# Kernel tuning notes

Hardware: AMD Instinct MI355X
Metric: run time of the kernel (lower is better)

The kernel has to match this reference:

```python
import jax, jax.numpy as jnp
import numpy as np

N = 50000      # nodes
E = 800000     # edges (avg degree 16)
F_IN = 128     # input feature dim
HID = 128      # 2 * out_classes
OUT = 64       # out_classes


def setup_inputs() -> dict:
    key = jax.random.key(0)
    ks = jax.random.split(key, 12)
    x = jax.random.normal(ks[0], (N, F_IN), jnp.float32)
    edge_index = jax.random.randint(ks[1], (2, E), 0, N, jnp.int32)
    def lin(k, fi, fo):
        return jax.random.normal(k, (fi, fo), jnp.float32) / np.float32(np.sqrt(fi))
    return {
        "x": x,
        "edge_index": edge_index,
        "W1": lin(ks[2], F_IN, HID), "b1": jnp.zeros((HID,), jnp.float32),
        "W2": lin(ks[3], HID, HID),  "b2": jnp.zeros((HID,), jnp.float32),
        "W3": lin(ks[4], HID, HID),  "b3": jnp.zeros((HID,), jnp.float32),
        "jk_w": jax.random.normal(ks[5], (3,), jnp.float32),
        "fc_W": lin(ks[6], HID, OUT), "fc_b": jnp.zeros((OUT,), jnp.float32),
    }


def _gcn_conv(h, W, b, row, col, n):
    """PyG GCNConv: linear -> add self-loops -> sym-normalized aggregate -> bias."""
    h = h @ W                                        # [n, d_out]
    loops = jnp.arange(n, dtype=row.dtype)
    r = jnp.concatenate([row, loops])                # sources
    c = jnp.concatenate([col, loops])                # targets
    deg = jax.ops.segment_sum(jnp.ones_like(c, h.dtype), c, num_segments=n)
    dinv = jnp.where(deg > 0, jax.lax.rsqrt(deg), 0.0)
    norm = dinv[r] * dinv[c]                         # [E+n]
    msg = h[r] * norm[:, None]                       # gather + scale
    return jax.ops.segment_sum(msg, c, num_segments=n) + b


def _neighbor_mean(h, row, col, n):
    """sample_neighbors with scale_factor=2: exact mean over out-neighbors,
    own feature when degree == 0 (top-k branch is provably dead code)."""
    s = jax.ops.segment_sum(h[col], row, num_segments=n)
    deg = jax.ops.segment_sum(jnp.ones_like(row, h.dtype), row, num_segments=n)
    mean = s / jnp.maximum(deg, 1.0)[:, None]
    return jnp.where((deg > 0)[:, None], mean, h)


def reference(x, edge_index, W1, b1, W2, b2, W3, b3, jk_w, fc_W, fc_b):
    row, col = edge_index[0], edge_index[1]
    n = x.shape[0]
    # layer 0: GCN -> ReLU -> (dropout: eval identity) -> neighbor sampling
    h0 = jax.nn.relu(_gcn_conv(x, W1, b1, row, col, n))
    h0 = _neighbor_mean(h0, row, col, n)
    # layer 1: GCN -> ReLU; historical-activation update is identity on first call
    h1 = jax.nn.relu(_gcn_conv(h0, W2, b2, row, col, n))
    # layer 2
    h2 = jax.nn.relu(_gcn_conv(h1, W3, b3, row, col, n))
    # dynamic JK aggregation
    w = jax.nn.softmax(jk_w)
    h = w[0] * h0 + w[1] * h1 + w[2] * h2
    return h @ fc_W + fc_b
```

## Files before the change

### kernel.cpp

```cpp
#include <hip/hip_runtime.h>
#include <stdint.h>

typedef unsigned int  uint32;
typedef unsigned short u16;

typedef short bfx8 __attribute__((ext_vector_type(8)));
typedef float f32x4 __attribute__((ext_vector_type(4)));
typedef float f32x2 __attribute__((ext_vector_type(2)));

#define NBP 256
#define CH  2048
#define BS  4608

__device__ __forceinline__ float b2f(u16 u) {
    union { uint32 i; float f; } v; v.i = ((uint32)u) << 16; return v.f;
}
__device__ __forceinline__ u16 f2b(float f) {
    union { float f; uint32 i; } v; v.f = f;
    uint32 u = v.i;
    return (u16)((u + 0x7fffu + ((u >> 16) & 1u)) >> 16);
}
__device__ __forceinline__ float blo(uint32 u) {
    union { uint32 i; float f; } v; v.i = u << 16; return v.f;
}
__device__ __forceinline__ float bhi(uint32 u) {
    union { uint32 i; float f; } v; v.i = u & 0xffff0000u; return v.f;
}
__device__ __forceinline__ uint32 packbf(float a, float b) {
    return (uint32)f2b(a) | ((uint32)f2b(b) << 16);
}
__device__ __forceinline__ void splitf(float x, u16& h, u16& l) {
    h = f2b(x);
    l = f2b(x - b2f(h));
}

__global__ __launch_bounds__(256) void k_init(
    int* __restrict__ curC, int* __restrict__ curR,
    const float* __restrict__ W1, const float* __restrict__ W2,
    const float* __restrict__ W3, const float* __restrict__ fcW,
    u16* __restrict__ WTh, u16* __restrict__ WTl, int WTN) {
    int t = threadIdx.x;
    if (blockIdx.x == 0) {
        curC[t] = t * BS;
        curR[t] = t * BS;
        return;
    }
    int i = ((int)blockIdx.x - 1) * 256 + t;
    if (i >= WTN) return;
    float w;
    if (i < 3 * 16384) {
        int m = i >> 14, j = i & 16383;
        int fo = j >> 7, fi = j & 127;
        const float* W = (m == 0) ? W1 : (m == 1) ? W2 : W3;
        w = W[fi * 128 + fo];
    } else {
        int j = i - 3 * 16384;
        int fo = j >> 7, fi = j & 127;
        w = fcW[fi * 64 + fo];
    }
    u16 h, l; splitf(w, h, l);
    WTh[i] = h; WTl[i] = l;
}

__global__ __launch_bounds__(256) void k_partC(
    const int* __restrict__ row, const int* __restrict__ col, int E,
    int* __restrict__ curC, int* __restrict__ curR,
    uint32* __restrict__ partC, uint32* __restrict__ partR) {
    __shared__ uint32 stagedC[CH], stagedR[CH];
    __shared__ int hp[NBP], expk[NBP], curp[NBP], runC[NBP], runR[NBP];
    __shared__ int wsum[4];
    int t = threadIdx.x;
    int lane = t & 63, wid = t >> 6;
    int base = blockIdx.x * CH;
    int n = E - base; if (n > CH) n = CH;

    int er[8], ec[8];
#pragma unroll
    for (int j = 0; j < 8; ++j) {
        int i = t + j * 256;
        if (i < n) { er[j] = row[base + i]; ec[j] = col[base + i]; }
        else er[j] = -1;
    }
    hp[t] = 0;
    __syncthreads();
#pragma unroll
    for (int j = 0; j < 8; ++j) {
        if (er[j] >= 0) {
            atomicAdd(&hp[ec[j] >> 8], 1);
            atomicAdd(&hp[er[j] >> 8], 0x10000);
        }
    }
    __syncthreads();
    int v = hp[t];
    int x = v;
#pragma unroll
    for (int d = 1; d < 64; d <<= 1) {
        int u = __shfl_up(x, d);
        if (lane >= d) x += u;
    }
    if (lane == 63) wsum[wid] = x;
    __syncthreads();
    int add = 0;
    for (int i = 0; i < wid; ++i) add += wsum[i];
    int ex = x + add - v;
    expk[t] = ex;
    curp[t] = ex;
    int vC = v & 0xffff, vR = v >> 16;
    runC[t] = vC ? atomicAdd(&curC[t], vC) : 0;
    runR[t] = vR ? atomicAdd(&curR[t], vR) : 0;
    __syncthreads();
#pragma unroll
    for (int j = 0; j < 8; ++j) {
        if (er[j] >= 0) {
            int cb = ec[j] >> 8, rb = er[j] >> 8;
            int pC = atomicAdd(&curp[cb], 1) & 0xffff;
            stagedC[pC] = ((uint32)ec[j] << 16) | (uint32)er[j];
            int pR = atomicAdd(&curp[rb], 0x10000) >> 16;
            stagedR[pR] = ((uint32)er[j] << 16) | (uint32)ec[j];
        }
    }
    __syncthreads();
    for (int i = t; i < n; i += 256) {
        uint32 pv = stagedC[i];
        int b = pv >> 24;
        partC[runC[b] + (i - (expk[b] & 0xffff))] = pv;
    }
    for (int i = t; i < n; i += 256) {
        uint32 pv = stagedR[i];
        int b = pv >> 24;
        partR[runR[b] + (i - (expk[b] >> 16))] = pv;
    }
}

__global__ __launch_bounds__(256) void k_fillD(
    const uint32* __restrict__ partC, const uint32* __restrict__ partR,
    const int* __restrict__ curC, const int* __restrict__ curR,
    int* __restrict__ off_in, int* __restrict__ end_in,
    int* __restrict__ off_out, int* __restrict__ end_out,
    u16* __restrict__ csr_src, u16* __restrict__ csr_dst,
    float* __restrict__ dinv, int NB, int N) {
    int part = ((int)blockIdx.x >= NB) ? 1 : 0;
    int b = (int)blockIdx.x - part * NB;
    const uint32* arr = part ? partR : partC;
    const int* curA   = part ? curR : curC;
    int* offA         = part ? off_out : off_in;
    int* endA         = part ? end_out : end_in;
    u16* csr          = part ? csr_dst : csr_src;
    int t = threadIdx.x;
    int lane = t & 63, wid = t >> 6;
    int base = b * BS, end = curA[b];
    __shared__ int cnt[NBP], cur[NBP];
    __shared__ int wsum[4];
    cnt[t] = 0;
    __syncthreads();
    for (int i = base + t; i < end; i += 256)
        atomicAdd(&cnt[(arr[i] >> 16) & 255], 1);
    __syncthreads();
    int v = cnt[t];
    int x = v;
#pragma unroll
    for (int d = 1; d < 64; d <<= 1) {
        int u = __shfl_up(x, d);
        if (lane >= d) x += u;
    }
    if (lane == 63) wsum[wid] = x;
    __syncthreads();
    int add = 0;
    for (int i = 0; i < wid; ++i) add += wsum[i];
    int ex = x + add - v;
    cur[t] = ex;
    int node = (b << 8) + t;
    if (node < N) {
        offA[node] = base + ex;
        endA[node] = base + ex + v;
        if (part == 0) dinv[node] = rsqrtf((float)(v + 1));
    }
    __syncthreads();
    for (int i = base + t; i < end; i += 256) {
        uint32 pv = arr[i];
        int local = (pv >> 16) & 255;
        int pos = atomicAdd(&cur[local], 1);
        csr[base + pos] = (u16)(pv & 0xffffu);
    }
}

__global__ __launch_bounds__(256) void k_gemm0(
    const float* __restrict__ A, const u16* __restrict__ WTh, const u16* __restrict__ WTl,
    const float* __restrict__ dinv, u16* __restrict__ G, int M) {
    const int lane = threadIdx.x & 63;
    const int q = lane >> 4, l = lane & 15;
    int rbase = blockIdx.x * 128 + (threadIdx.x >> 6) * 32;
    if (rbase >= M) return;
    int r0 = rbase + l;      if (r0 >= M) r0 = M - 1;
    int r1 = rbase + 16 + l; if (r1 >= M) r1 = M - 1;

    f32x4 acc[2][8];
#pragma unroll
    for (int i = 0; i < 2; ++i)
#pragma unroll
        for (int j = 0; j < 8; ++j) acc[i][j] = (f32x4){0.f, 0.f, 0.f, 0.f};

#pragma unroll
    for (int kc = 0; kc < 4; ++kc) {
        int k0 = kc * 32 + q * 8;
        bfx8 ah0, ah1;
        {
            f32x4 a = *(const f32x4*)(A + (size_t)r0 * 128 + k0);
            f32x4 b = *(const f32x4*)(A + (size_t)r0 * 128 + k0 + 4);
            float xx[8] = {a[0], a[1], a[2], a[3], b[0], b[1], b[2], b[3]};
#pragma unroll
            for (int j = 0; j < 8; ++j) ah0[j] = (short)f2b(xx[j]);
        }
        {
            f32x4 a = *(const f32x4*)(A + (size_t)r1 * 128 + k0);
            f32x4 b = *(const f32x4*)(A + (size_t)r1 * 128 + k0 + 4);
            float xx[8] = {a[0], a[1], a[2], a[3], b[0], b[1], b[2], b[3]};
#pragma unroll
            for (int j = 0; j < 8; ++j) ah1[j] = (short)f2b(xx[j]);
        }
#pragma unroll
        for (int ct = 0; ct < 8; ++ct) {
            bfx8 bh = *(const bfx8*)(WTh + (ct * 16 + l) * 128 + k0);
            bfx8 bl = *(const bfx8*)(WTl + (ct * 16 + l) * 128 + k0);
            acc[0][ct] = __builtin_amdgcn_mfma_f32_16x16x32_bf16(ah0, bh, acc[0][ct], 0, 0, 0);
            acc[0][ct] = __builtin_amdgcn_mfma_f32_16x16x32_bf16(ah0, bl, acc[0][ct], 0, 0, 0);
            acc[1][ct] = __builtin_amdgcn_mfma_f32_16x16x32_bf16(ah1, bh, acc[1][ct], 0, 0, 0);
            acc[1][ct] = __builtin_amdgcn_mfma_f32_16x16x32_bf16(ah1, bl, acc[1][ct], 0, 0, 0);
        }
    }
#pragma unroll
    for (int rs = 0; rs < 2; ++rs) {
#pragma unroll
        for (int rr = 0; rr < 4; ++rr) {
            int rw = rbase + rs * 16 + q * 4 + rr;
            if (rw < M) {
                float dv = dinv[rw];
#pragma unroll
                for (int ct = 0; ct < 8; ++ct)
                    G[(size_t)rw * 128 + ct * 16 + l] = f2b(acc[rs][ct][rr] * dv);
            }
        }
    }
}

__global__ __launch_bounds__(256) void k_gemm1p(
    const u16* __restrict__ Ah,
    const u16* __restrict__ WTh, const u16* __restrict__ WTl,
    const float* __restrict__ dinv, u16* __restrict__ G, int M) {
    const int lane = threadIdx.x & 63;
    const int q = lane >> 4, l = lane & 15;
    int rbase = blockIdx.x * 128 + (threadIdx.x >> 6) * 32;
    if (rbase >= M) return;
    int r0 = rbase + l;      if (r0 >= M) r0 = M - 1;
    int r1 = rbase + 16 + l; if (r1 >= M) r1 = M - 1;

    f32x4 acc[2][8];
#pragma unroll
    for (int i = 0; i < 2; ++i)
#pragma unroll
        for (int j = 0; j < 8; ++j) acc[i][j] = (f32x4){0.f, 0.f, 0.f, 0.f};

#pragma unroll
    for (int kc = 0; kc < 4; ++kc) {
        int k0 = kc * 32 + q * 8;
        bfx8 ah0 = *(const bfx8*)(Ah + (size_t)r0 * 128 + k0);
        bfx8 ah1 = *(const bfx8*)(Ah + (size_t)r1 * 128 + k0);
#pragma unroll
        for (int ct = 0; ct < 8; ++ct) {
            bfx8 bh = *(const bfx8*)(WTh + (ct * 16 + l) * 128 + k0);
            bfx8 bl = *(const bfx8*)(WTl + (ct * 16 + l) * 128 + k0);
            acc[0][ct] = __builtin_amdgcn_mfma_f32_16x16x32_bf16(ah0, bh, acc[0][ct], 0, 0, 0);
            acc[0][ct] = __builtin_amdgcn_mfma_f32_16x16x32_bf16(ah0, bl, acc[0][ct], 0, 0, 0);
            acc[1][ct] = __builtin_amdgcn_mfma_f32_16x16x32_bf16(ah1, bh, acc[1][ct], 0, 0, 0);
            acc[1][ct] = __builtin_amdgcn_mfma_f32_16x16x32_bf16(ah1, bl, acc[1][ct], 0, 0, 0);
        }
    }
#pragma unroll
    for (int rs = 0; rs < 2; ++rs) {
#pragma unroll
        for (int rr = 0; rr < 4; ++rr) {
            int rw = rbase + rs * 16 + q * 4 + rr;
            if (rw < M) {
                float dv = dinv[rw];
#pragma unroll
                for (int ct = 0; ct < 8; ++ct)
                    G[(size_t)rw * 128 + ct * 16 + l] = f2b(acc[rs][ct][rr] * dv);
            }
        }
    }
}

__global__ __launch_bounds__(256) void k_agg(
    const uint32* __restrict__ g, const u16* __restrict__ csr,
    const int* __restrict__ off, const int* __restrict__ endo,
    const float* __restrict__ dinv,
    const f32x2* __restrict__ bias, uint32* __restrict__ outH, int n) {
    int w = (blockIdx.x * 256 + threadIdx.x) >> 6;
    if (w >= n) return;
    int lane = threadIdx.x & 63;
    uint32 sv = g[(size_t)w * 64 + lane];
    float s0 = blo(sv), s1 = bhi(sv);
    int e = off[w], e1 = endo[w];
    for (; e + 16 <= e1; e += 16) {
        int ix[16];
#pragma unroll
        for (int j = 0; j < 16; ++j) ix[j] = csr[e + j];
        uint32 vv[16];
#pragma unroll
        for (int j = 0; j < 16; ++j) vv[j] = g[(size_t)ix[j] * 64 + lane];
#pragma unroll
        for (int j = 0; j < 16; ++j) { s0 += blo(vv[j]); s1 += bhi(vv[j]); }
    }
    for (; e + 4 <= e1; e += 4) {
        int ix[4];
#pragma unroll
        for (int j = 0; j < 4; ++j) ix[j] = csr[e + j];
        uint32 vv[4];
#pragma unroll
        for (int j = 0; j < 4; ++j) vv[j] = g[(size_t)ix[j] * 64 + lane];
#pragma unroll
        for (int j = 0; j < 4; ++j) { s0 += blo(vv[j]); s1 += bhi(vv[j]); }
    }
    for (; e < e1; ++e) {
        uint32 v = g[(size_t)csr[e] * 64 + lane];
        s0 += blo(v); s1 += bhi(v);
    }
    float dc = dinv[w];
    f32x2 bb = bias[lane];
    float o0 = fmaxf(fmaf(s0, dc, bb[0]), 0.f);
    float o1 = fmaxf(fmaf(s1, dc, bb[1]), 0.f);
    outH[(size_t)w * 64 + lane] = packbf(o0, o1);
}

__global__ __launch_bounds__(256) void k_mean(
    const uint32* __restrict__ h, const u16* __restrict__ csr,
    const int* __restrict__ off, const int* __restrict__ endo,
    uint32* __restrict__ outH, int n) {
    int w = (blockIdx.x * 256 + threadIdx.x) >> 6;
    if (w >= n) return;
    int lane = threadIdx.x & 63;
    int e = off[w], e1 = endo[w];
    int d = e1 - e;
    float s0 = 0.f, s1 = 0.f;
    for (; e + 16 <= e1; e += 16) {
        int ix[16];
#pragma unroll
        for (int j = 0; j < 16; ++j) ix[j] = csr[e + j];
        uint32 vv[16];
#pragma unroll
        for (int j = 0; j < 16; ++j) vv[j] = h[(size_t)ix[j] * 64 + lane];
#pragma unroll
        for (int j = 0; j < 16; ++j) { s0 += blo(vv[j]); s1 += bhi(vv[j]); }
    }
    for (; e + 4 <= e1; e += 4) {
        int ix[4];
#pragma unroll
        for (int j = 0; j < 4; ++j) ix[j] = csr[e + j];
        uint32 vv[4];
#pragma unroll
        for (int j = 0; j < 4; ++j) vv[j] = h[(size_t)ix[j] * 64 + lane];
#pragma unroll
        for (int j = 0; j < 4; ++j) { s0 += blo(vv[j]); s1 += bhi(vv[j]); }
    }
    for (; e < e1; ++e) {
        uint32 v = h[(size_t)csr[e] * 64 + lane];
        s0 += blo(v); s1 += bhi(v);
    }
    float o0, o1;
    if (d > 0) {
        float inv = 1.f / (float)d;
        o0 = s0 * inv; o1 = s1 * inv;
    } else {
        uint32 sv = h[(size_t)w * 64 + lane];
        o0 = blo(sv); o1 = bhi(sv);
    }
    outH[(size_t)w * 64 + lane] = packbf(o0, o1);
}

__global__ __launch_bounds__(256) void k_final(
    const u16* __restrict__ h0, const u16* __restrict__ h1,
    const u16* __restrict__ h2, const float* __restrict__ jkw,
    const u16* __restrict__ fcWTh, const u16* __restrict__ fcWTl,
    const float* __restrict__ fcb, float* __restrict__ out, int M) {
    float a0 = jkw[0], a1 = jkw[1], a2 = jkw[2];
    float mx = fmaxf(a0, fmaxf(a1, a2));
    float e0 = expf(a0 - mx), e1 = expf(a1 - mx), e2 = expf(a2 - mx);
    float inv = 1.f / (e0 + e1 + e2);
    float w0 = e0 * inv, w1 = e1 * inv, w2 = e2 * inv;

    const int lane = threadIdx.x & 63;
    const int q = lane >> 4, l = lane & 15;
    int rbase = blockIdx.x * 128 + (threadIdx.x >> 6) * 32;
    if (rbase >= M) return;
    int r0 = rbase + l;      if (r0 >= M) r0 = M - 1;
    int r1 = rbase + 16 + l; if (r1 >= M) r1 = M - 1;

    f32x4 acc[2][4];
#pragma unroll
    for (int i = 0; i < 2; ++i)
#pragma unroll
        for (int j = 0; j < 4; ++j) acc[i][j] = (f32x4){0.f, 0.f, 0.f, 0.f};

    union U8 { bfx8 v; u16 u[8]; };

#pragma unroll
    for (int kc = 0; kc < 4; ++kc) {
        int k0 = kc * 32 + q * 8;
        bfx8 ah[2];
        const int rr2[2] = {r0, r1};
#pragma unroll
        for (int half = 0; half < 2; ++half) {
            size_t o = (size_t)rr2[half] * 128 + k0;
            U8 x0, x1, x2, rh;
            x0.v = *(const bfx8*)(h0 + o);
            x1.v = *(const bfx8*)(h1 + o);
            x2.v = *(const bfx8*)(h2 + o);
#pragma unroll
            for (int j = 0; j < 8; ++j) {
                float c = w0 * b2f(x0.u[j]) + w1 * b2f(x1.u[j]) + w2 * b2f(x2.u[j]);
                rh.u[j] = f2b(c);
            }
            ah[half] = rh.v;
        }
#pragma unroll
        for (int ct = 0; ct < 4; ++ct) {
            bfx8 bh = *(const bfx8*)(fcWTh + (ct * 16 + l) * 128 + k0);
            bfx8 bl = *(const bfx8*)(fcWTl + (ct * 16 + l) * 128 + k0);
#pragma unroll
            for (int half = 0; half < 2; ++half) {
                acc[half][ct] = __builtin_amdgcn_mfma_f32_16x16x32_bf16(ah[half], bh, acc[half][ct], 0, 0, 0);
                acc[half][ct] = __builtin_amdgcn_mfma_f32_16x16x32_bf16(ah[half], bl, acc[half][ct], 0, 0, 0);
            }
        }
    }
#pragma unroll
    for (int rs = 0; rs < 2; ++rs) {
#pragma unroll
        for (int rr = 0; rr < 4; ++rr) {
            int rw = rbase + rs * 16 + q * 4 + rr;
            if (rw < M) {
#pragma unroll
                for (int ct = 0; ct < 4; ++ct) {
                    int cc = ct * 16 + l;
                    out[(size_t)rw * 64 + cc] = acc[rs][ct][rr] + fcb[cc];
                }
            }
        }
    }
}

extern "C" void kernel_launch(void* const* d_in, const int* in_sizes, int n_in,
                              void* d_out, int out_size, void* d_ws, size_t ws_size,
                              hipStream_t stream) {
    const int N = in_sizes[0] / 128;
    const int E = in_sizes[1] / 2;
    const int NB = (N + 255) >> 8;

    const float* x    = (const float*)d_in[0];
    const int* row    = (const int*)d_in[1];
    const int* col    = row + E;
    const float* W1   = (const float*)d_in[2];
    const float* b1   = (const float*)d_in[3];
    const float* W2   = (const float*)d_in[4];
    const float* b2   = (const float*)d_in[5];
    const float* W3   = (const float*)d_in[6];
    const float* b3   = (const float*)d_in[7];
    const float* jkw  = (const float*)d_in[8];
    const float* fcW  = (const float*)d_in[9];
    const float* fcb  = (const float*)d_in[10];
    float* outp       = (float*)d_out;

    char* ws = (char*)d_ws;
    size_t off = 0;
    auto alloc = [&](size_t bytes) -> char* {
        char* p = ws + off;
        off += (bytes + 255) & ~(size_t)255;
        return p;
    };
    int* curC   = (int*)alloc((size_t)NBP * sizeof(int));
    int* curR   = (int*)alloc((size_t)NBP * sizeof(int));
    int* off_in  = (int*)alloc((size_t)N * sizeof(int));
    int* end_in  = (int*)alloc((size_t)N * sizeof(int));
    int* off_out = (int*)alloc((size_t)N * sizeof(int));
    int* end_out = (int*)alloc((size_t)N * sizeof(int));
    uint32* partC = (uint32*)alloc((size_t)NBP * BS * sizeof(uint32));
    uint32* partR = (uint32*)alloc((size_t)NBP * BS * sizeof(uint32));
    u16* csr_src = (u16*)alloc((size_t)NBP * BS * sizeof(u16));
    u16* csr_dst = (u16*)alloc((size_t)NBP * BS * sizeof(u16));
    float* dinv  = (float*)alloc((size_t)N * sizeof(float));
    const int WTN = 3 * 16384 + 8192;
    u16* WTh = (u16*)alloc((size_t)WTN * sizeof(u16));
    u16* WTl = (u16*)alloc((size_t)WTN * sizeof(u16));
    size_t FB = (size_t)N * 128 * sizeof(u16);
    u16* gbuf = (u16*)alloc(FB);
    u16* t0   = (u16*)alloc(FB);
    u16* h0   = (u16*)alloc(FB);
    u16* h1   = (u16*)alloc(FB);
    u16* h2   = (u16*)alloc(FB);

    const int B = 256;
    int Gh = (E + CH - 1) / CH;
    int Gg = (N + 127) / 128;
    int Gwt = (WTN + B - 1) / B;

    k_init<<<1 + Gwt, B, 0, stream>>>(curC, curR, W1, W2, W3, fcW, WTh, WTl, WTN);
    k_partC<<<Gh, B, 0, stream>>>(row, col, E, curC, curR, partC, partR);
    k_fillD<<<2 * NB, B, 0, stream>>>(partC, partR, curC, curR,
                                      off_in, end_in, off_out, end_out,
                                      csr_src, csr_dst, dinv, NB, N);
    k_gemm0<<<Gg, B, 0, stream>>>(x, WTh, WTl, dinv, gbuf, N);

    int aggG = (N + 3) / 4;

    k_agg<<<aggG, B, 0, stream>>>((const uint32*)gbuf, csr_src, off_in, end_in, dinv,
                                  (const f32x2*)b1, (uint32*)t0, N);
    k_mean<<<aggG, B, 0, stream>>>((const uint32*)t0, csr_dst, off_out, end_out,
                                   (uint32*)h0, N);
    k_gemm1p<<<Gg, B, 0, stream>>>(h0, WTh + 16384, WTl + 16384, dinv, gbuf, N);
    k_agg<<<aggG, B, 0, stream>>>((const uint32*)gbuf, csr_src, off_in, end_in, dinv,
                                  (const f32x2*)b2, (uint32*)h1, N);
    k_gemm1p<<<Gg, B, 0, stream>>>(h1, WTh + 2 * 16384, WTl + 2 * 16384, dinv, gbuf, N);
    k_agg<<<aggG, B, 0, stream>>>((const uint32*)gbuf, csr_src, off_in, end_in, dinv,
                                  (const f32x2*)b3, (uint32*)h2, N);
    k_final<<<Gg, B, 0, stream>>>(h0, h1, h2, jkw,
                                  WTh + 3 * 16384, WTl + 3 * 16384, fcb, outp, N);
}
```

Baseline: 335.2 us.

## Fuse GCN aggregation with following GEMMs and merge setup kernels

Merges the weight-split init into the edge partition kernel and the first GEMM into the CSR fill kernel. The first GEMM runs concurrently with CSR construction, so it no longer scales by dinv; the first aggregation applies per-neighbor dinv instead. The mean, aggregation and final JK/fc steps are fused with the next layer's GEMM through a 16-row shared-memory tile, cutting the launch count and the round trips of intermediate features through memory. The cost is extra dinv gathers per edge in the first aggregation and small per-block GEMMs that reload weights in every block, plus a memset to zero the bucket cursors.

```diff
diff --git a/kernel.cpp b/kernel.cpp
--- a/kernel.cpp
+++ b/kernel.cpp
@@ -34,42 +34,35 @@
     l = f2b(x - b2f(h));
 }
 
-__global__ __launch_bounds__(256) void k_init(
+__global__ __launch_bounds__(256) void k_partC_ws(
+    const int* __restrict__ row, const int* __restrict__ col, int E, int Gh,
     int* __restrict__ curC, int* __restrict__ curR,
+    uint32* __restrict__ partC, uint32* __restrict__ partR,
     const float* __restrict__ W1, const float* __restrict__ W2,
     const float* __restrict__ W3, const float* __restrict__ fcW,
     u16* __restrict__ WTh, u16* __restrict__ WTl, int WTN) {
-    int t = threadIdx.x;
-    if (blockIdx.x == 0) {
-        curC[t] = t * BS;
-        curR[t] = t * BS;
-        return;
-    }
-    int i = ((int)blockIdx.x - 1) * 256 + t;
-    if (i >= WTN) return;
-    float w;
-    if (i < 3 * 16384) {
-        int m = i >> 14, j = i & 16383;
-        int fo = j >> 7, fi = j & 127;
-        const float* W = (m == 0) ? W1 : (m == 1) ? W2 : W3;
-        w = W[fi * 128 + fo];
-    } else {
-        int j = i - 3 * 16384;
-        int fo = j >> 7, fi = j & 127;
-        w = fcW[fi * 64 + fo];
-    }
-    u16 h, l; splitf(w, h, l);
-    WTh[i] = h; WTl[i] = l;
-}
-
-__global__ __launch_bounds__(256) void k_partC(
-    const int* __restrict__ row, const int* __restrict__ col, int E,
-    int* __restrict__ curC, int* __restrict__ curR,
-    uint32* __restrict__ partC, uint32* __restrict__ partR) {
     __shared__ uint32 stagedC[CH], stagedR[CH];
     __shared__ int hp[NBP], expk[NBP], curp[NBP], runC[NBP], runR[NBP];
     __shared__ int wsum[4];
     int t = threadIdx.x;
+    if ((int)blockIdx.x >= Gh) {
+        int i = ((int)blockIdx.x - Gh) * 256 + t;
+        if (i >= WTN) return;
+        float w;
+        if (i < 3 * 16384) {
+            int m = i >> 14, j = i & 16383;
+            int fo = j >> 7, fi = j & 127;
+            const float* W = (m == 0) ? W1 : (m == 1) ? W2 : W3;
+            w = W[fi * 128 + fo];
+        } else {
+            int j = i - 3 * 16384;
+            int fo = j >> 7, fi = j & 127;
+            w = fcW[fi * 64 + fo];
+        }
+        u16 h, l; splitf(w, h, l);
+        WTh[i] = h; WTl[i] = l;
+        return;
+    }
     int lane = t & 63, wid = t >> 6;
     int base = blockIdx.x * CH;
     int n = E - base; if (n > CH) n = CH;
@@ -106,8 +99,8 @@
     expk[t] = ex;
     curp[t] = ex;
     int vC = v & 0xffff, vR = v >> 16;
-    runC[t] = vC ? atomicAdd(&curC[t], vC) : 0;
-    runR[t] = vR ? atomicAdd(&curR[t], vR) : 0;
+    runC[t] = t * BS + (vC ? atomicAdd(&curC[t], vC) : 0);
+    runR[t] = t * BS + (vR ? atomicAdd(&curR[t], vR) : 0);
     __syncthreads();
 #pragma unroll
     for (int j = 0; j < 8; ++j) {
@@ -132,13 +125,70 @@
     }
 }
 
-__global__ __launch_bounds__(256) void k_fillD(
+__global__ __launch_bounds__(256) void k_fillD_g0(
     const uint32* __restrict__ partC, const uint32* __restrict__ partR,
     const int* __restrict__ curC, const int* __restrict__ curR,
     int* __restrict__ off_in, int* __restrict__ end_in,
     int* __restrict__ off_out, int* __restrict__ end_out,
     u16* __restrict__ csr_src, u16* __restrict__ csr_dst,
-    float* __restrict__ dinv, int NB, int N) {
+    float* __restrict__ dinv, int NB, int N,
+    const float* __restrict__ A, const u16* __restrict__ WTh,
+    const u16* __restrict__ WTl, u16* __restrict__ G) {
+    if ((int)blockIdx.x >= 2 * NB) {
+        int blk = (int)blockIdx.x - 2 * NB;
+        const int lane = threadIdx.x & 63;
+        const int q = lane >> 4, l = lane & 15;
+        int rbase = blk * 128 + (threadIdx.x >> 6) * 32;
+        if (rbase >= N) return;
+        int r0 = rbase + l;      if (r0 >= N) r0 = N - 1;
+        int r1 = rbase + 16 + l; if (r1 >= N) r1 = N - 1;
+        f32x4 acc[2][8];
+#pragma unroll
+        for (int i = 0; i < 2; ++i)
+#pragma unroll
+            for (int j = 0; j < 8; ++j) acc[i][j] = (f32x4){0.f, 0.f, 0.f, 0.f};
+#pragma unroll
+        for (int kc = 0; kc < 4; ++kc) {
+            int k0 = kc * 32 + q * 8;
+            bfx8 ah0, ah1;
+            {
+                f32x4 a = *(const f32x4*)(A + (size_t)r0 * 128 + k0);
+                f32x4 b = *(const f32x4*)(A + (size_t)r0 * 128 + k0 + 4);
+                float xx[8] = {a[0], a[1], a[2], a[3], b[0], b[1], b[2], b[3]};
+#pragma unroll
+                for (int j = 0; j < 8; ++j) ah0[j] = (short)f2b(xx[j]);
+            }
+            {
+                f32x4 a = *(const f32x4*)(A + (size_t)r1 * 128 + k0);
+                f32x4 b = *(const f32x4*)(A + (size_t)r1 * 128 + k0 + 4);
+                float xx[8] = {a[0], a[1], a[2], a[3], b[0], b[1], b[2], b[3]};
+#pragma unroll
+                for (int j = 0; j < 8; ++j) ah1[j] = (short)f2b(xx[j]);
+            }
+#pragma unroll
+            for (int ct = 0; ct < 8; ++ct) {
+                bfx8 bh = *(const bfx8*)(WTh + (ct * 16 + l) * 128 + k0);
+                bfx8 bl = *(const bfx8*)(WTl + (ct * 16 + l) * 128 + k0);
+                acc[0][ct] = __builtin_amdgcn_mfma_f32_16x16x32_bf16(ah0, bh, acc[0][ct], 0, 0, 0);
+                acc[0][ct] = __builtin_amdgcn_mfma_f32_16x16x32_bf16(ah0, bl, acc[0][ct], 0, 0, 0);
+                acc[1][ct] = __builtin_amdgcn_mfma_f32_16x16x32_bf16(ah1, bh, acc[1][ct], 0, 0, 0);
+                acc[1][ct] = __builtin_amdgcn_mfma_f32_16x16x32_bf16(ah1, bl, acc[1][ct], 0, 0, 0);
+            }
+        }
+#pragma unroll
+        for (int rs = 0; rs < 2; ++rs) {
+#pragma unroll
+            for (int rr = 0; rr < 4; ++rr) {
+                int rw = rbase + rs * 16 + q * 4 + rr;
+                if (rw < N) {
+#pragma unroll
+                    for (int ct = 0; ct < 8; ++ct)
+                        G[(size_t)rw * 128 + ct * 16 + l] = f2b(acc[rs][ct][rr]);
+                }
+            }
+        }
+        return;
+    }
     int part = ((int)blockIdx.x >= NB) ? 1 : 0;
     int b = (int)blockIdx.x - part * NB;
     const uint32* arr = part ? partR : partC;
@@ -148,7 +198,7 @@
     u16* csr          = part ? csr_dst : csr_src;
     int t = threadIdx.x;
     int lane = t & 63, wid = t >> 6;
-    int base = b * BS, end = curA[b];
+    int base = b * BS, end = base + curA[b];
     __shared__ int cnt[NBP], cur[NBP];
     __shared__ int wsum[4];
     cnt[t] = 0;
@@ -184,113 +234,7 @@
     }
 }
 
-__global__ __launch_bounds__(256) void k_gemm0(
-    const float* __restrict__ A, const u16* __restrict__ WTh, const u16* __restrict__ WTl,
-    const float* __restrict__ dinv, u16* __restrict__ G, int M) {
-    const int lane = threadIdx.x & 63;
-    const int q = lane >> 4, l = lane & 15;
-    int rbase = blockIdx.x * 128 + (threadIdx.x >> 6) * 32;
-    if (rbase >= M) return;
-    int r0 = rbase + l;      if (r0 >= M) r0 = M - 1;
-    int r1 = rbase + 16 + l; if (r1 >= M) r1 = M - 1;
-
-    f32x4 acc[2][8];
-#pragma unroll
-    for (int i = 0; i < 2; ++i)
-#pragma unroll
-        for (int j = 0; j < 8; ++j) acc[i][j] = (f32x4){0.f, 0.f, 0.f, 0.f};
-
-#pragma unroll
-    for (int kc = 0; kc < 4; ++kc) {
-        int k0 = kc * 32 + q * 8;
-        bfx8 ah0, ah1;
-        {
-            f32x4 a = *(const f32x4*)(A + (size_t)r0 * 128 + k0);
-            f32x4 b = *(const f32x4*)(A + (size_t)r0 * 128 + k0 + 4);
-            float xx[8] = {a[0], a[1], a[2], a[3], b[0], b[1], b[2], b[3]};
-#pragma unroll
-            for (int j = 0; j < 8; ++j) ah0[j] = (short)f2b(xx[j]);
-        }
-        {
-            f32x4 a = *(const f32x4*)(A + (size_t)r1 * 128 + k0);
-            f32x4 b = *(const f32x4*)(A + (size_t)r1 * 128 + k0 + 4);
-            float xx[8] = {a[0], a[1], a[2], a[3], b[0], b[1], b[2], b[3]};
-#pragma unroll
-            for (int j = 0; j < 8; ++j) ah1[j] = (short)f2b(xx[j]);
-        }
-#pragma unroll
-        for (int ct = 0; ct < 8; ++ct) {
-            bfx8 bh = *(const bfx8*)(WTh + (ct * 16 + l) * 128 + k0);
-            bfx8 bl = *(const bfx8*)(WTl + (ct * 16 + l) * 128 + k0);
-            acc[0][ct] = __builtin_amdgcn_mfma_f32_16x16x32_bf16(ah0, bh, acc[0][ct], 0, 0, 0);
-            acc[0][ct] = __builtin_amdgcn_mfma_f32_16x16x32_bf16(ah0, bl, acc[0][ct], 0, 0, 0);
-            acc[1][ct] = __builtin_amdgcn_mfma_f32_16x16x32_bf16(ah1, bh, acc[1][ct], 0, 0, 0);
-            acc[1][ct] = __builtin_amdgcn_mfma_f32_16x16x32_bf16(ah1, bl, acc[1][ct], 0, 0, 0);
-        }
-    }
-#pragma unroll
-    for (int rs = 0; rs < 2; ++rs) {
-#pragma unroll
-        for (int rr = 0; rr < 4; ++rr) {
-            int rw = rbase + rs * 16 + q * 4 + rr;
-            if (rw < M) {
-                float dv = dinv[rw];
-#pragma unroll
-                for (int ct = 0; ct < 8; ++ct)
-                    G[(size_t)rw * 128 + ct * 16 + l] = f2b(acc[rs][ct][rr] * dv);
-            }
-        }
-    }
-}
-
-__global__ __launch_bounds__(256) void k_gemm1p(
-    const u16* __restrict__ Ah,
-    const u16* __restrict__ WTh, const u16* __restrict__ WTl,
-    const float* __restrict__ dinv, u16* __restrict__ G, int M) {
-    const int lane = threadIdx.x & 63;
-    const int q = lane >> 4, l = lane & 15;
-    int rbase = blockIdx.x * 128 + (threadIdx.x >> 6) * 32;
-    if (rbase >= M) return;
-    int r0 = rbase + l;      if (r0 >= M) r0 = M - 1;
-    int r1 = rbase + 16 + l; if (r1 >= M) r1 = M - 1;
-
-    f32x4 acc[2][8];
-#pragma unroll
-    for (int i = 0; i < 2; ++i)
-#pragma unroll
-        for (int j = 0; j < 8; ++j) acc[i][j] = (f32x4){0.f, 0.f, 0.f, 0.f};
-
-#pragma unroll
-    for (int kc = 0; kc < 4; ++kc) {
-        int k0 = kc * 32 + q * 8;
-        bfx8 ah0 = *(const bfx8*)(Ah + (size_t)r0 * 128 + k0);
-        bfx8 ah1 = *(const bfx8*)(Ah + (size_t)r1 * 128 + k0);
-#pragma unroll
-        for (int ct = 0; ct < 8; ++ct) {
-            bfx8 bh = *(const bfx8*)(WTh + (ct * 16 + l) * 128 + k0);
-            bfx8 bl = *(const bfx8*)(WTl + (ct * 16 + l) * 128 + k0);
-            acc[0][ct] = __builtin_amdgcn_mfma_f32_16x16x32_bf16(ah0, bh, acc[0][ct], 0, 0, 0);
-            acc[0][ct] = __builtin_amdgcn_mfma_f32_16x16x32_bf16(ah0, bl, acc[0][ct], 0, 0, 0);
-            acc[1][ct] = __builtin_amdgcn_mfma_f32_16x16x32_bf16(ah1, bh, acc[1][ct], 0, 0, 0);
-            acc[1][ct] = __builtin_amdgcn_mfma_f32_16x16x32_bf16(ah1, bl, acc[1][ct], 0, 0, 0);
-        }
-    }
-#pragma unroll
-    for (int rs = 0; rs < 2; ++rs) {
-#pragma unroll
-        for (int rr = 0; rr < 4; ++rr) {
-            int rw = rbase + rs * 16 + q * 4 + rr;
-            if (rw < M) {
-                float dv = dinv[rw];
-#pragma unroll
-                for (int ct = 0; ct < 8; ++ct)
-                    G[(size_t)rw * 128 + ct * 16 + l] = f2b(acc[rs][ct][rr] * dv);
-            }
-        }
-    }
-}
-
-__global__ __launch_bounds__(256) void k_agg(
+__global__ __launch_bounds__(256) void k_agg0(
     const uint32* __restrict__ g, const u16* __restrict__ csr,
     const int* __restrict__ off, const int* __restrict__ endo,
     const float* __restrict__ dinv,
@@ -298,8 +242,9 @@
     int w = (blockIdx.x * 256 + threadIdx.x) >> 6;
     if (w >= n) return;
     int lane = threadIdx.x & 63;
+    float dc = dinv[w];
     uint32 sv = g[(size_t)w * 64 + lane];
-    float s0 = blo(sv), s1 = bhi(sv);
+    float s0 = blo(sv) * dc, s1 = bhi(sv) * dc;
     int e = off[w], e1 = endo[w];
     for (; e + 16 <= e1; e += 16) {
         int ix[16];
@@ -308,47 +253,38 @@
         uint32 vv[16];
 #pragma unroll
         for (int j = 0; j < 16; ++j) vv[j] = g[(size_t)ix[j] * 64 + lane];
-#pragma unroll
-        for (int j = 0; j < 16; ++j) { s0 += blo(vv[j]); s1 += bhi(vv[j]); }
-    }
-    for (; e + 4 <= e1; e += 4) {
-        int ix[4];
-#pragma unroll
-        for (int j = 0; j < 4; ++j) ix[j] = csr[e + j];
-        uint32 vv[4];
-#pragma unroll
-        for (int j = 0; j < 4; ++j) vv[j] = g[(size_t)ix[j] * 64 + lane];
-#pragma unroll
-        for (int j = 0; j < 4; ++j) { s0 += blo(vv[j]); s1 += bhi(vv[j]); }
+        float dm[16];
+#pragma unroll
+        for (int j = 0; j < 16; ++j) dm[j] = dinv[ix[j]];
+#pragma unroll
+        for (int j = 0; j < 16; ++j) {
+            s0 = fmaf(blo(vv[j]), dm[j], s0);
+            s1 = fmaf(bhi(vv[j]), dm[j], s1);
+        }
     }
     for (; e < e1; ++e) {
-        uint32 v = g[(size_t)csr[e] * 64 + lane];
-        s0 += blo(v); s1 += bhi(v);
-    }
-    float dc = dinv[w];
+        int ix = csr[e];
+        uint32 v = g[(size_t)ix * 64 + lane];
+        float dm = dinv[ix];
+        s0 = fmaf(blo(v), dm, s0);
+        s1 = fmaf(bhi(v), dm, s1);
+    }
     f32x2 bb = bias[lane];
     float o0 = fmaxf(fmaf(s0, dc, bb[0]), 0.f);
     float o1 = fmaxf(fmaf(s1, dc, bb[1]), 0.f);
     outH[(size_t)w * 64 + lane] = packbf(o0, o1);
 }
 
-__global__ __launch_bounds__(256) void k_mean(
-    const uint32* __restrict__ h, const u16* __restrict__ csr,
-    const int* __restrict__ off, const int* __restrict__ endo,
-    uint32* __restrict__ outH, int n) {
-    int w = (blockIdx.x * 256 + threadIdx.x) >> 6;
-    if (w >= n) return;
-    int lane = threadIdx.x & 63;
-    int e = off[w], e1 = endo[w];
-    int d = e1 - e;
-    float s0 = 0.f, s1 = 0.f;
+__device__ __forceinline__ void gather_sum(
+    const uint32* __restrict__ g, const u16* __restrict__ csr,
+    int e, int e1, int lane, float& s0, float& s1) {
     for (; e + 16 <= e1; e += 16) {
         int ix[16];
 #pragma unroll
         for (int j = 0; j < 16; ++j) ix[j] = csr[e + j];
         uint32 vv[16];
 #pragma unroll
-        for (int j = 0; j < 16; ++j) vv[j] = h[(size_t)ix[j] * 64 + lane];
+        for (int j = 0; j < 16; ++j) vv[j] = g[(size_t)ix[j] * 64 + lane];
 #pragma unroll
         for (int j = 0; j < 16; ++j) { s0 += blo(vv[j]); s1 += bhi(vv[j]); }
     }
@@ -358,94 +294,165 @@
         for (int j = 0; j < 4; ++j) ix[j] = csr[e + j];
         uint32 vv[4];
 #pragma unroll
-        for (int j = 0; j < 4; ++j) vv[j] = h[(size_t)ix[j] * 64 + lane];
+        for (int j = 0; j < 4; ++j) vv[j] = g[(size_t)ix[j] * 64 + lane];
 #pragma unroll
         for (int j = 0; j < 4; ++j) { s0 += blo(vv[j]); s1 += bhi(vv[j]); }
     }
     for (; e < e1; ++e) {
-        uint32 v = h[(size_t)csr[e] * 64 + lane];
+        uint32 v = g[(size_t)csr[e] * 64 + lane];
         s0 += blo(v); s1 += bhi(v);
     }
-    float o0, o1;
-    if (d > 0) {
-        float inv = 1.f / (float)d;
-        o0 = s0 * inv; o1 = s1 * inv;
-    } else {
-        uint32 sv = h[(size_t)w * 64 + lane];
-        o0 = blo(sv); o1 = bhi(sv);
-    }
-    outH[(size_t)w * 64 + lane] = packbf(o0, o1);
-}
-
-__global__ __launch_bounds__(256) void k_final(
-    const u16* __restrict__ h0, const u16* __restrict__ h1,
-    const u16* __restrict__ h2, const float* __restrict__ jkw,
+}
+
+__device__ __forceinline__ void tile_gemm128(
+    const u16* __restrict__ tile,
+    const u16* __restrict__ WTh, const u16* __restrict__ WTl,
+    const float* __restrict__ dinv, u16* __restrict__ G, int nbase, int N,
+    int wv, int lane) {
+    const int q = lane >> 4, l = lane & 15;
+    f32x4 acc[2];
+    acc[0] = (f32x4){0.f, 0.f, 0.f, 0.f};
+    acc[1] = (f32x4){0.f, 0.f, 0.f, 0.f};
+#pragma unroll
+    for (int kc = 0; kc < 4; ++kc) {
+        bfx8 a = *(const bfx8*)(tile + l * 136 + kc * 32 + q * 8);
+#pragma unroll
+        for (int c = 0; c < 2; ++c) {
+            int ct = 2 * wv + c;
+            bfx8 bh = *(const bfx8*)(WTh + (ct * 16 + l) * 128 + kc * 32 + q * 8);
+            bfx8 bl = *(const bfx8*)(WTl + (ct * 16 + l) * 128 + kc * 32 + q * 8);
+            acc[c] = __builtin_amdgcn_mfma_f32_16x16x32_bf16(a, bh, acc[c], 0, 0, 0);
+            acc[c] = __builtin_amdgcn_mfma_f32_16x16x32_bf16(a, bl, acc[c], 0, 0, 0);
+        }
+    }
+#pragma unroll
+    for (int rr = 0; rr < 4; ++rr) {
+        int rw = nbase + q * 4 + rr;
+        if (rw < N) {
+            float dv = dinv[rw];
+#pragma unroll
+            for (int c = 0; c < 2; ++c)
+                G[(size_t)rw * 128 + (2 * wv + c) * 16 + l] = f2b(acc[c][rr] * dv);
+        }
+    }
+}
+
+__global__ __launch_bounds__(256) void k_meangemm1(
+    const uint32* __restrict__ t0, const u16* __restrict__ csr,
+    const int* __restrict__ off, const int* __restrict__ endo,
+    uint32* __restrict__ h0, const u16* __restrict__ WTh, const u16* __restrict__ WTl,
+    const float* __restrict__ dinv, u16* __restrict__ G, int N) {
+    __shared__ u16 tile[16 * 136];
+    int t = threadIdx.x;
+    int wv = t >> 6, lane = t & 63;
+    int nbase = blockIdx.x * 16;
+#pragma unroll
+    for (int k = 0; k < 4; ++k) {
+        int r = nbase + wv * 4 + k;
+        bool valid = (r < N);
+        int rc = valid ? r : N - 1;
+        int e = off[rc], e1 = endo[rc];
+        int deg = e1 - e;
+        float s0 = 0.f, s1 = 0.f;
+        gather_sum(t0, csr, e, e1, lane, s0, s1);
+        float o0, o1;
+        if (deg > 0) {
+            float inv = 1.f / (float)deg;
+            o0 = s0 * inv; o1 = s1 * inv;
+        } else {
+            uint32 sv = t0[(size_t)rc * 64 + lane];
+            o0 = blo(sv); o1 = bhi(sv);
+        }
+        uint32 pk = packbf(o0, o1);
+        ((uint32*)tile)[(wv * 4 + k) * 68 + lane] = pk;
+        if (valid) h0[(size_t)r * 64 + lane] = pk;
+    }
+    __syncthreads();
+    tile_gemm128(tile, WTh, WTl, dinv, G, nbase, N, wv, lane);
+}
+
+__global__ __launch_bounds__(256) void k_agggemm2(
+    const uint32* __restrict__ gA, const u16* __restrict__ csr,
+    const int* __restrict__ off, const int* __restrict__ endo,
+    const float* __restrict__ dinv, const f32x2* __restrict__ bias,
+    uint32* __restrict__ h1, const u16* __restrict__ WTh, const u16* __restrict__ WTl,
+    u16* __restrict__ G, int N) {
+    __shared__ u16 tile[16 * 136];
+    int t = threadIdx.x;
+    int wv = t >> 6, lane = t & 63;
+    int nbase = blockIdx.x * 16;
+    f32x2 bb = bias[lane];
+#pragma unroll
+    for (int k = 0; k < 4; ++k) {
+        int r = nbase + wv * 4 + k;
+        bool valid = (r < N);
+        int rc = valid ? r : N - 1;
+        uint32 sv = gA[(size_t)rc * 64 + lane];
+        float s0 = blo(sv), s1 = bhi(sv);
+        gather_sum(gA, csr, off[rc], endo[rc], lane, s0, s1);
+        float dc = dinv[rc];
+        float o0 = fmaxf(fmaf(s0, dc, bb[0]), 0.f);
+        float o1 = fmaxf(fmaf(s1, dc, bb[1]), 0.f);
+        uint32 pk = packbf(o0, o1);
+        ((uint32*)tile)[(wv * 4 + k) * 68 + lane] = pk;
+        if (valid) h1[(size_t)r * 64 + lane] = pk;
+    }
+    __syncthreads();
+    tile_gemm128(tile, WTh, WTl, dinv, G, nbase, N, wv, lane);
+}
+
+__global__ __launch_bounds__(256) void k_aggfinal(
+    const uint32* __restrict__ gB, const u16* __restrict__ csr,
+    const int* __restrict__ off, const int* __restrict__ endo,
+    const float* __restrict__ dinv, const f32x2* __restrict__ bias,
+    const uint32* __restrict__ h0, const uint32* __restrict__ h1,
+    const float* __restrict__ jkw,
     const u16* __restrict__ fcWTh, const u16* __restrict__ fcWTl,
-    const float* __restrict__ fcb, float* __restrict__ out, int M) {
+    const float* __restrict__ fcb, float* __restrict__ out, int N) {
+    __shared__ u16 tile[16 * 136];
     float a0 = jkw[0], a1 = jkw[1], a2 = jkw[2];
     float mx = fmaxf(a0, fmaxf(a1, a2));
-    float e0 = expf(a0 - mx), e1 = expf(a1 - mx), e2 = expf(a2 - mx);
-    float inv = 1.f / (e0 + e1 + e2);
-    float w0 = e0 * inv, w1 = e1 * inv, w2 = e2 * inv;
-
-    const int lane = threadIdx.x & 63;
+    float e0 = expf(a0 - mx), e1x = expf(a1 - mx), e2 = expf(a2 - mx);
+    float inv = 1.f / (e0 + e1x + e2);
+    float w0 = e0 * inv, w1 = e1x * inv, w2 = e2 * inv;
+
+    int t = threadIdx.x;
+    int wv = t >> 6, lane = t & 63;
+    int nbase = blockIdx.x * 16;
+    f32x2 bb = bias[lane];
+#pragma unroll
+    for (int k = 0; k < 4; ++k) {
+        int r = nbase + wv * 4 + k;
+        int rc = (r < N) ? r : N - 1;
+        uint32 sv = gB[(size_t)rc * 64 + lane];
+        float s0 = blo(sv), s1 = bhi(sv);
+        gather_sum(gB, csr, off[rc], endo[rc], lane, s0, s1);
+        float dc = dinv[rc];
+        float o0 = fmaxf(fmaf(s0, dc, bb[0]), 0.f);
+        float o1 = fmaxf(fmaf(s1, dc, bb[1]), 0.f);
+        uint32 v0 = h0[(size_t)rc * 64 + lane];
+        uint32 v1 = h1[(size_t)rc * 64 + lane];
+        float c0 = w0 * blo(v0) + w1 * blo(v1) + w2 * o0;
+        float c1 = w0 * bhi(v0) + w1 * bhi(v1) + w2 * o1;
+        ((uint32*)tile)[(wv * 4 + k) * 68 + lane] = packbf(c0, c1);
+    }
+    __syncthreads();
     const int q = lane >> 4, l = lane & 15;
-    int rbase = blockIdx.x * 128 + (threadIdx.x >> 6) * 32;
-    if (rbase >= M) return;
-    int r0 = rbase + l;      if (r0 >= M) r0 = M - 1;
-    int r1 = rbase + 16 + l; if (r1 >= M) r1 = M - 1;
-
-    f32x4 acc[2][4];
-#pragma unroll
-    for (int i = 0; i < 2; ++i)
-#pragma unroll
-        for (int j = 0; j < 4; ++j) acc[i][j] = (f32x4){0.f, 0.f, 0.f, 0.f};
-
-    union U8 { bfx8 v; u16 u[8]; };
-
+    f32x4 acc = (f32x4){0.f, 0.f, 0.f, 0.f};
 #pragma unroll
     for (int kc = 0; kc < 4; ++kc) {
-        int k0 = kc * 32 + q * 8;
-        bfx8 ah[2];
-        const int rr2[2] = {r0, r1};
-#pragma unroll
-        for (int half = 0; half < 2; ++half) {
-            size_t o = (size_t)rr2[half] * 128 + k0;
-            U8 x0, x1, x2, rh;
-            x0.v = *(const bfx8*)(h0 + o);
-            x1.v = *(const bfx8*)(h1 + o);
-            x2.v = *(const bfx8*)(h2 + o);
-#pragma unroll
-            for (int j = 0; j < 8; ++j) {
-                float c = w0 * b2f(x0.u[j]) + w1 * b2f(x1.u[j]) + w2 * b2f(x2.u[j]);
-                rh.u[j] = f2b(c);
-            }
-            ah[half] = rh.v;
-        }
-#pragma unroll
-        for (int ct = 0; ct < 4; ++ct) {
-            bfx8 bh = *(const bfx8*)(fcWTh + (ct * 16 + l) * 128 + k0);
-            bfx8 bl = *(const bfx8*)(fcWTl + (ct * 16 + l) * 128 + k0);
-#pragma unroll
-            for (int half = 0; half < 2; ++half) {
-                acc[half][ct] = __builtin_amdgcn_mfma_f32_16x16x32_bf16(ah[half], bh, acc[half][ct], 0, 0, 0);
-                acc[half][ct] = __builtin_amdgcn_mfma_f32_16x16x32_bf16(ah[half], bl, acc[half][ct], 0, 0, 0);
-            }
-        }
-    }
-#pragma unroll
-    for (int rs = 0; rs < 2; ++rs) {
-#pragma unroll
-        for (int rr = 0; rr < 4; ++rr) {
-            int rw = rbase + rs * 16 + q * 4 + rr;
-            if (rw < M) {
-#pragma unroll
-                for (int ct = 0; ct < 4; ++ct) {
-                    int cc = ct * 16 + l;
-                    out[(size_t)rw * 64 + cc] = acc[rs][ct][rr] + fcb[cc];
-                }
-            }
-        }
+        bfx8 a = *(const bfx8*)(tile + l * 136 + kc * 32 + q * 8);
+        bfx8 bh = *(const bfx8*)(fcWTh + (wv * 16 + l) * 128 + kc * 32 + q * 8);
+        bfx8 bl = *(const bfx8*)(fcWTl + (wv * 16 + l) * 128 + kc * 32 + q * 8);
+        acc = __builtin_amdgcn_mfma_f32_16x16x32_bf16(a, bh, acc, 0, 0, 0);
+        acc = __builtin_amdgcn_mfma_f32_16x16x32_bf16(a, bl, acc, 0, 0, 0);
+    }
+    float fb = fcb[wv * 16 + l];
+#pragma unroll
+    for (int rr = 0; rr < 4; ++rr) {
+        int rw = nbase + q * 4 + rr;
+        if (rw < N)
+            out[(size_t)rw * 64 + wv * 16 + l] = acc[rr] + fb;
     }
 }
 
@@ -477,8 +484,8 @@
         off += (bytes + 255) & ~(size_t)255;
         return p;
     };
-    int* curC   = (int*)alloc((size_t)NBP * sizeof(int));
-    int* curR   = (int*)alloc((size_t)NBP * sizeof(int));
+    int* curC   = (int*)alloc((size_t)2 * NBP * sizeof(int));
+    int* curR   = curC + NBP;
     int* off_in  = (int*)alloc((size_t)N * sizeof(int));
     int* end_in  = (int*)alloc((size_t)N * sizeof(int));
     int* off_out = (int*)alloc((size_t)N * sizeof(int));
@@ -492,36 +499,38 @@
     u16* WTh = (u16*)alloc((size_t)WTN * sizeof(u16));
     u16* WTl = (u16*)alloc((size_t)WTN * sizeof(u16));
     size_t FB = (size_t)N * 128 * sizeof(u16);
-    u16* gbuf = (u16*)alloc(FB);
-    u16* t0   = (u16*)alloc(FB);
-    u16* h0   = (u16*)alloc(FB);
-    u16* h1   = (u16*)alloc(FB);
-    u16* h2   = (u16*)alloc(FB);
+    u16* g0 = (u16*)alloc(FB);
+    u16* t0 = (u16*)alloc(FB);
+    u16* h0 = (u16*)alloc(FB);
+    u16* h1 = (u16*)alloc(FB);
+    u16* gA = (u16*)alloc(FB);
+    u16* gB = (u16*)alloc(FB);
+
+    hipMemsetAsync(curC, 0, (size_t)2 * NBP * sizeof(int), stream);
 
     const int B = 256;
     int Gh = (E + CH - 1) / CH;
     int Gg = (N + 127) / 128;
     int Gwt = (WTN + B - 1) / B;
-
-    k_init<<<1 + Gwt, B, 0, stream>>>(curC, curR, W1, W2, W3, fcW, WTh, WTl, WTN);
-    k_partC<<<Gh, B, 0, stream>>>(row, col, E, curC, curR, partC, partR);
-    k_fillD<<<2 * NB, B, 0, stream>>>(partC, partR, curC, curR,
-                                      off_in, end_in, off_out, end_out,
-                                      csr_src, csr_dst, dinv, NB, N);
-    k_gemm0<<<Gg, B, 0, stream>>>(x, WTh, WTl, dinv, gbuf, N);
-
+    int Gf = (N + 15) / 16;
+
+    k_partC_ws<<<Gh + Gwt, B, 0, stream>>>(row, col, E, Gh, curC, curR, partC, partR,
+                                           W1, W2, W3, fcW, WTh, WTl, WTN);
+    k_fillD_g0<<<2 * NB + Gg, B, 0, stream>>>(partC, partR, curC, curR,
+                                              off_in, end_in, off_out, end_out,
+                                              csr_src, csr_dst, dinv, NB, N,
+                                              x, WTh, WTl, g0);
     int aggG = (N + 3) / 4;
-
-    k_agg<<<aggG, B, 0, stream>>>((const uint32*)gbuf, csr_src, off_in, end_in, dinv,
-                                  (const f32x2*)b1, (uint32*)t0, N);
-    k_mean<<<aggG, B, 0, stream>>>((const uint32*)t0, csr_dst, off_out, end_out,
-                                   (uint32*)h0, N);
-    k_gemm1p<<<Gg, B, 0, stream>>>(h0, WTh + 16384, WTl + 16384, dinv, gbuf, N);
-    k_agg<<<aggG, B, 0, stream>>>((const uint32*)gbuf, csr_src, off_in, end_in, dinv,
-                                  (const f32x2*)b2, (uint32*)h1, N);
-    k_gemm1p<<<Gg, B, 0, stream>>>(h1, WTh + 2 * 16384, WTl + 2 * 16384, dinv, gbuf, N);
-    k_agg<<<aggG, B, 0, stream>>>((const uint32*)gbuf, csr_src, off_in, end_in, dinv,
-                                  (const f32x2*)b3, (uint32*)h2, N);
-    k_final<<<Gg, B, 0, stream>>>(h0, h1, h2, jkw,
-                                  WTh + 3 * 16384, WTl + 3 * 16384, fcb, outp, N);
-}
+    k_agg0<<<aggG, B, 0, stream>>>((const uint32*)g0, csr_src, off_in, end_in, dinv,
+                                   (const f32x2*)b1, (uint32*)t0, N);
+    k_meangemm1<<<Gf, B, 0, stream>>>((const uint32*)t0, csr_dst, off_out, end_out,
+                                      (uint32*)h0, WTh + 16384, WTl + 16384,
+                                      dinv, gA, N);
+    k_agggemm2<<<Gf, B, 0, stream>>>((const uint32*)gA, csr_src, off_in, end_in,
+                                     dinv, (const f32x2*)b2, (uint32*)h1,
+                                     WTh + 2 * 16384, WTl + 2 * 16384, gB, N);
+    k_aggfinal<<<Gf, B, 0, stream>>>((const uint32*)gB, csr_src, off_in, end_in,
+                                     dinv, (const f32x2*)b3,
+                                     (const uint32*)h0, (const uint32*)h1, jkw,
+                                     WTh + 3 * 16384, WTl + 3 * 16384, fcb, outp, N);
+}
```

New measurement: 359.5 us. 7.2% more time.
